# Performance work log

Hardware: AMD Instinct MI355X
Metric: run time of the kernel (lower is better)

Reference implementation:

```python
import jax, jax.numpy as jnp
import numpy as np

RADIUS = 0.12
K = 32  # neighbors per ball


def setup_inputs() -> dict:
    key = jax.random.key(0)
    ks = jax.random.split(key, 12)
    B, N, M, C = 4, 4096, 4096, 128
    anchor_xyzs = jax.random.uniform(ks[0], (B, N, 3), dtype=jnp.float32)
    neighbor = jax.random.uniform(ks[1], (B, M, 3), dtype=jnp.float32)
    s3 = 1.0 / np.sqrt(3.0)
    sC = 1.0 / np.sqrt(C)
    Wq = jax.random.uniform(ks[2], (3, C), jnp.float32, -s3, s3)
    bq = jax.random.uniform(ks[3], (C,), jnp.float32, -s3, s3)
    Wk = jax.random.uniform(ks[4], (3, C), jnp.float32, -s3, s3)
    bk = jax.random.uniform(ks[5], (C,), jnp.float32, -s3, s3)
    Wd = jax.random.uniform(ks[6], (3, C), jnp.float32, -s3, s3)
    bd = jax.random.uniform(ks[7], (C,), jnp.float32, -s3, s3)
    Wa = jax.random.uniform(ks[8], (C, C), jnp.float32, -sC, sC)
    ba = jax.random.uniform(ks[9], (C,), jnp.float32, -sC, sC)
    return {"anchor_xyzs": anchor_xyzs, "neighbor": neighbor,
            "Wq": Wq, "bq": bq, "Wk": Wk, "bk": bk,
            "Wd": Wd, "bd": bd, "Wa": Wa, "ba": ba}


def ball_query(anchor, neighbor, radius, k):
    """pointnet2-style ball query: first k neighbor indices (in original order)
    with sqdist < radius^2; slots beyond the found count are padded with the
    first found index (index 0 if none found). Returns (B, N, k) int32."""
    # (B, N, M) pairwise squared distances
    sqd = jnp.sum((anchor[:, :, None, :] - neighbor[:, None, :, :]) ** 2, axis=-1)
    mask = sqd < radius * radius
    # stable sort keys: valid (0) before invalid (1) -> first-k valid indices in order
    order = jnp.argsort((~mask).astype(jnp.int32), axis=-1, stable=True)
    idx = order[..., :k]                                # (B, N, k)
    cnt = jnp.sum(mask, axis=-1)                        # (B, N)
    slot_valid = jnp.arange(k) < cnt[..., None]
    idx = jnp.where(slot_valid, idx, idx[..., :1])
    return idx.astype(jnp.int32)


def reference(anchor_xyzs, neighbor, Wq, bq, Wk, bk, Wd, bd, Wa, ba):
    B, N, _ = anchor_xyzs.shape
    bidx = jnp.arange(B)[:, None, None]
    # QKV-style projections of coordinates
    Q = anchor_xyzs @ Wq + bq                           # (B, N, C)
    neighbor_k = neighbor @ Wk + bk                     # (B, M, C)
    # ball query + gather
    idx = ball_query(anchor_xyzs, neighbor, RADIUS, K)  # (B, N, K)
    neighbor_grouped = neighbor[bidx, idx]              # (B, N, K, 3)
    features_K = neighbor_k[bidx, idx]                  # (B, N, K, C)
    # distance encoding
    dis = (anchor_xyzs[:, :, None, :] - neighbor_grouped) @ Wd + bd  # (B, N, K, C)
    # attention weight: softmax over channel dim (dim=-1, as in the torch code)
    logits = (Q[:, :, None, :] - features_K) @ Wa + ba  # (B, N, K, C)
    attention_weight = jax.nn.softmax(logits, axis=-1)
    # max-pool over the K neighbor axis
    attention = jnp.max(dis * attention_weight, axis=2)  # (B, N, C)
    return attention
```

## Files before the change

kernel.cpp:

```cpp
#include <hip/hip_runtime.h>
#include <math.h>

#define BDIM 4
#define NDIM 4096
#define MDIM 4096
#define CDIM 128
#define KSEL 32
#define NCELL 64
#define CAP 128

typedef float v2f __attribute__((ext_vector_type(2)));

#define PRE_BYTES (7 * CDIM * 4)
#define STARTS_BYTES ((NCELL + 1) * BDIM * 4)
#define PTS4_OFF (PRE_BYTES + STARTS_BYTES)
#define WS_NEEDED (PTS4_OFF + (size_t)BDIM * MDIM * 16)

template <int CTRL, int MASK>
__device__ __forceinline__ float dpp_add(float x) {
    const int r = __builtin_amdgcn_update_dpp(0, __float_as_int(x), CTRL, MASK, 0xF, true);
    return x + __int_as_float(r);
}
#define DPP_QUAD_XOR1 0xB1
#define DPP_QUAD_XOR2 0x4E
#define DPP_ROW_HALF_MIRROR 0x141
#define DPP_ROW_MIRROR      0x140
#define DPP_ROW_BCAST15     0x142
#define DPP_ROW_BCAST31     0x143

__device__ __forceinline__ int cell_of(float v) {
    int c = (int)(v * 4.0f);
    return c < 0 ? 0 : (c > 3 ? 3 : c);
}

__launch_bounds__(1024)
__global__ void setup_kernel(const float* __restrict__ neighbor,
                             const float* __restrict__ Wq, const float* __restrict__ bq,
                             const float* __restrict__ Wk, const float* __restrict__ bk,
                             const float* __restrict__ Wa, const float* __restrict__ ba,
                             float* __restrict__ pre,
                             int* __restrict__ starts,
                             float4* __restrict__ pts4,
                             const int do_bins) {
    const int blk = blockIdx.x;
    const int t = threadIdx.x;
    if (do_bins && blk < BDIM) {
        __shared__ int cnts[NCELL];
        __shared__ int curs[NCELL];
        if (t < NCELL) cnts[t] = 0;
        __syncthreads();
        const float* nbb = neighbor + (size_t)blk * MDIM * 3;
        float px[4], py[4], pz[4];
        int cell[4];
        #pragma unroll
        for (int k = 0; k < 4; ++k) {
            const int i = t + k * 1024;
            const float x = nbb[3 * i], y = nbb[3 * i + 1], z = nbb[3 * i + 2];
            px[k] = x; py[k] = y; pz[k] = z;
            cell[k] = (cell_of(z) * 4 + cell_of(y)) * 4 + cell_of(x);
            atomicAdd(&cnts[cell[k]], 1);
        }
        __syncthreads();
        if (t < NCELL) {
            const int v = cnts[t];
            int inc = v;
            #pragma unroll
            for (int off = 1; off < 64; off <<= 1) {
                const int u = __shfl_up(inc, off);
                if (t >= off) inc += u;
            }
            const int excl = inc - v;
            curs[t] = excl;
            starts[blk * (NCELL + 1) + t] = excl;
            if (t == NCELL - 1) starts[blk * (NCELL + 1) + NCELL] = inc;
        }
        __syncthreads();
        #pragma unroll
        for (int k = 0; k < 4; ++k) {
            const int i = t + k * 1024;
            const int slot = atomicAdd(&curs[cell[k]], 1);
            pts4[(size_t)blk * MDIM + slot] = make_float4(px[k], py[k], pz[k], __int_as_float(i));
        }
    } else if (!do_bins || blk == BDIM) {
        if (t < 7 * CDIM) {
            const double LOG2E = 1.4426950408889634074;
            const int r = t >> 7, c = t & (CDIM - 1);
            if (r < 3) {
                double s0 = 0, s1 = 0, s2 = 0, s3 = 0;
                for (int k = 0; k < CDIM; k += 4) {
                    s0 += (double)Wq[r * CDIM + k + 0] * (double)Wa[(k + 0) * CDIM + c];
                    s1 += (double)Wq[r * CDIM + k + 1] * (double)Wa[(k + 1) * CDIM + c];
                    s2 += (double)Wq[r * CDIM + k + 2] * (double)Wa[(k + 2) * CDIM + c];
                    s3 += (double)Wq[r * CDIM + k + 3] * (double)Wa[(k + 3) * CDIM + c];
                }
                pre[r * CDIM + c] = (float)(((s0 + s1) + (s2 + s3)) * LOG2E);
            } else if (r < 6) {
                const int rr = r - 3;
                double s0 = 0, s1 = 0, s2 = 0, s3 = 0;
                for (int k = 0; k < CDIM; k += 4) {
                    s0 += (double)Wk[rr * CDIM + k + 0] * (double)Wa[(k + 0) * CDIM + c];
                    s1 += (double)Wk[rr * CDIM + k + 1] * (double)Wa[(k + 1) * CDIM + c];
                    s2 += (double)Wk[rr * CDIM + k + 2] * (double)Wa[(k + 2) * CDIM + c];
                    s3 += (double)Wk[rr * CDIM + k + 3] * (double)Wa[(k + 3) * CDIM + c];
                }
                pre[r * CDIM + c] = (float)(((s0 + s1) + (s2 + s3)) * LOG2E);
            } else {
                double s = (double)ba[c];
                for (int k = 0; k < CDIM; ++k)
                    s += ((double)bq[k] - (double)bk[k]) * (double)Wa[k * CDIM + c];
                pre[6 * CDIM + c] = (float)(s * LOG2E);
            }
        }
    }
}

__launch_bounds__(256)
__global__ void attn2_kernel(const float* __restrict__ anchor,
                             const float* __restrict__ neighbor,
                             const float* __restrict__ Wd,
                             const float* __restrict__ bd,
                             const float* __restrict__ pre,
                             const float4* __restrict__ pts4,
                             const int* __restrict__ starts,
                             float* __restrict__ out) {
    __shared__ float4 cand[4][CAP];
    __shared__ float4 sel[4][KSEL];

    const int b    = blockIdx.x >> 10;
    const int n0   = (blockIdx.x & 1023) << 2;
    const int tid  = threadIdx.x;
    const int w    = tid >> 6;
    const int lane = tid & 63;

    const int n = n0 + w;
    const float* ap = anchor + ((size_t)b * NDIM + n) * 3;
    const float ax = ap[0], ay = ap[1], az = ap[2];
    const float* nbb = neighbor + (size_t)b * MDIM * 3;

    const v2f* pre2 = (const v2f*)pre;
    const v2f* wdp  = (const v2f*)Wd;
    const v2f* bdp  = (const v2f*)bd;
    const v2f wqa0 = pre2[0 * 64 + lane], wqa1 = pre2[1 * 64 + lane], wqa2 = pre2[2 * 64 + lane];
    const v2f wka0 = pre2[3 * 64 + lane], wka1 = pre2[4 * 64 + lane], wka2 = pre2[5 * 64 + lane];
    const v2f cav  = pre2[6 * 64 + lane];
    const v2f wd0 = wdp[0 * 64 + lane], wd1 = wdp[1 * 64 + lane], wd2 = wdp[2 * 64 + lane];
    const v2f bdv = bdp[lane];

    const v2f qa = ax * wqa0 + ay * wqa1 + az * wqa2 + cav;
    const v2f ad = ax * wd0 + ay * wd1 + az * wd2 + bdv;

    constexpr float R2 = (float)(0.12 * 0.12);
    const float RP = 0.1201f;
    const unsigned long long lanelt = (1ull << lane) - 1ull;

    const int cx0 = max(0, (int)((ax - RP) * 4.0f)), cx1 = min(3, (int)((ax + RP) * 4.0f));
    const int cy0 = max(0, (int)((ay - RP) * 4.0f)), cy1 = min(3, (int)((ay + RP) * 4.0f));
    const int cz0 = max(0, (int)((az - RP) * 4.0f)), cz1 = min(3, (int)((az + RP) * 4.0f));

    const float4* pb = pts4 + (size_t)b * MDIM;
    const int* st = starts + b * (NCELL + 1);

    int rs[4], re[4];
    int nr = 0;
    for (int cz = cz0; cz <= cz1; ++cz)
        for (int cy = cy0; cy <= cy1; ++cy) {
            const int crow = (cz * 4 + cy) * 4;
            rs[nr] = st[crow + cx0];
            re[nr] = st[crow + cx1 + 1];
            ++nr;
        }

    int cnt = 0;
    for (int r = 0; r < nr; ++r) {
        const int rend = re[r];
        for (int base = rs[r]; base < rend; base += 64) {
            const int i = base + lane;
            const bool valid = i < rend;
            float4 p = make_float4(1e30f, 1e30f, 1e30f, 0.0f);
            if (valid) p = pb[i];
            const float dx = __fsub_rn(ax, p.x);
            const float dy = __fsub_rn(ay, p.y);
            const float dz = __fsub_rn(az, p.z);
            const float d2 = __fadd_rn(__fadd_rn(__fmul_rn(dx, dx), __fmul_rn(dy, dy)),
                                       __fmul_rn(dz, dz));
            const bool in = valid && (d2 < R2);
            const unsigned long long mk = __ballot(in);
            const int pos = cnt + __popcll(mk & lanelt);
            if (in && pos < CAP) cand[w][pos] = p;
            cnt += __popcll(mk);
        }
    }

    int eff;
    if (cnt == 0) {
        if (lane == 0) sel[w][0] = make_float4(nbb[0], nbb[1], nbb[2], __int_as_float(0));
        eff = 1;
    } else if (cnt <= KSEL) {
        if (lane < cnt) sel[w][lane] = cand[w][lane];
        eff = cnt;
    } else if (cnt <= CAP) {
        float4 c0v = make_float4(0, 0, 0, 0), c1v = make_float4(0, 0, 0, 0);
        int i0 = 0x7fffffff, i1 = 0x7fffffff;
        if (lane < cnt)      { c0v = cand[w][lane];      i0 = __float_as_int(c0v.w); }
        if (lane + 64 < cnt) { c1v = cand[w][lane + 64]; i1 = __float_as_int(c1v.w); }
        int lo = 0, hi = MDIM - 1;
        while (lo < hi) {
            const int mid = (lo + hi) >> 1;
            const int c = __popcll(__ballot(i0 <= mid)) + __popcll(__ballot(i1 <= mid));
            if (c >= KSEL) hi = mid; else lo = mid + 1;
        }
        const bool k0 = (i0 <= lo);
        const unsigned long long m0 = __ballot(k0);
        if (k0) sel[w][__popcll(m0 & lanelt)] = c0v;
        const int cc0 = __popcll(m0);
        const bool k1 = (i1 <= lo);
        const unsigned long long m1 = __ballot(k1);
        if (k1) sel[w][cc0 + __popcll(m1 & lanelt)] = c1v;
        eff = KSEL;
    } else {
        int c2 = 0;
        for (int base = 0; base < MDIM && c2 < KSEL; base += 64) {
            const int m = base + lane;
            const float* p = nbb + 3 * m;
            const float nx = p[0], ny = p[1], nz = p[2];
            const float dx = __fsub_rn(ax, nx);
            const float dy = __fsub_rn(ay, ny);
            const float dz = __fsub_rn(az, nz);
            const float d2 = __fadd_rn(__fadd_rn(__fmul_rn(dx, dx), __fmul_rn(dy, dy)),
                                       __fmul_rn(dz, dz));
            const bool in = d2 < R2;
            const unsigned long long mk = __ballot(in);
            const int pos = c2 + __popcll(mk & lanelt);
            if (in && pos < KSEL) sel[w][pos] = make_float4(nx, ny, nz, 0.0f);
            c2 += __popcll(mk);
        }
        eff = KSEL;
    }

    const int eff4 = (eff + 3) & ~3;
    __builtin_amdgcn_wave_barrier();
    __builtin_amdgcn_s_waitcnt(0);
    if (lane >= eff && lane < eff4) {
        const float4 f = sel[w][0];
        sel[w][lane] = f;
    }
    __builtin_amdgcn_wave_barrier();

    v2f acc = { -1e30f, -1e30f };
    for (int j = 0; j < eff4; j += 4) {
        v2f pr[4];
        float sv[4];
        #pragma unroll
        for (int t = 0; t < 4; ++t) {
            const float4 v = sel[w][j + t];
            const v2f l = qa - (v.x * wka0 + v.y * wka1 + v.z * wka2);
            v2f e; e.x = exp2f(l.x); e.y = exp2f(l.y);
            sv[t] = e.x + e.y;
            const v2f d = ad - (v.x * wd0 + v.y * wd1 + v.z * wd2);
            pr[t] = d * e;
        }
        #pragma unroll
        for (int t = 0; t < 4; ++t) sv[t] = dpp_add<DPP_QUAD_XOR1, 0xF>(sv[t]);
        #pragma unroll
        for (int t = 0; t < 4; ++t) sv[t] = dpp_add<DPP_QUAD_XOR2, 0xF>(sv[t]);
        #pragma unroll
        for (int t = 0; t < 4; ++t) sv[t] = dpp_add<DPP_ROW_HALF_MIRROR, 0xF>(sv[t]);
        #pragma unroll
        for (int t = 0; t < 4; ++t) sv[t] = dpp_add<DPP_ROW_MIRROR, 0xF>(sv[t]);
        #pragma unroll
        for (int t = 0; t < 4; ++t) sv[t] = dpp_add<DPP_ROW_BCAST15, 0xA>(sv[t]);
        #pragma unroll
        for (int t = 0; t < 4; ++t) sv[t] = dpp_add<DPP_ROW_BCAST31, 0xC>(sv[t]);
        #pragma unroll
        for (int t = 0; t < 4; ++t) {
            const float tot = __int_as_float(__builtin_amdgcn_readlane(__float_as_int(sv[t]), 63));
            const float inv = __builtin_amdgcn_rcpf(tot);
            const v2f c = pr[t] * inv;
            acc.x = fmaxf(acc.x, c.x);
            acc.y = fmaxf(acc.y, c.y);
        }
    }

    float2 o; o.x = acc.x; o.y = acc.y;
    ((float2*)out)[((size_t)b * NDIM + n) * 64 + lane] = o;
}

__launch_bounds__(256)
__global__ void attn_fallback(const float* __restrict__ anchor,
                              const float* __restrict__ neighbor,
                              const float* __restrict__ Wd,
                              const float* __restrict__ bd,
                              const float* __restrict__ pre,
                              float* __restrict__ out) {
    __shared__ int    lists[4][KSEL];
    __shared__ float4 nxyz[4][KSEL];

    const int b = blockIdx.x >> 10, n0 = (blockIdx.x & 1023) << 2;
    const int tid = threadIdx.x, w = tid >> 6, lane = tid & 63;
    const int n = n0 + w;
    const float* ap = anchor + ((size_t)b * NDIM + n) * 3;
    const float ax = ap[0], ay = ap[1], az = ap[2];
    const float* nbb = neighbor + (size_t)b * MDIM * 3;

    const v2f* pre2 = (const v2f*)pre;
    const v2f* wdp = (const v2f*)Wd;
    const v2f* bdp = (const v2f*)bd;
    const v2f wqa0 = pre2[0 * 64 + lane], wqa1 = pre2[1 * 64 + lane], wqa2 = pre2[2 * 64 + lane];
    const v2f wka0 = pre2[3 * 64 + lane], wka1 = pre2[4 * 64 + lane], wka2 = pre2[5 * 64 + lane];
    const v2f cav = pre2[6 * 64 + lane];
    const v2f wd0 = wdp[0 * 64 + lane], wd1 = wdp[1 * 64 + lane], wd2 = wdp[2 * 64 + lane];
    const v2f bdv = bdp[lane];
    const v2f qa = ax * wqa0 + ay * wqa1 + az * wqa2 + cav;
    const v2f ad = ax * wd0 + ay * wd1 + az * wd2 + bdv;

    constexpr float R2 = (float)(0.12 * 0.12);
    const unsigned long long lanelt = (1ull << lane) - 1ull;
    int cnt = 0;
    for (int base = 0; base < MDIM && cnt < KSEL; base += 64) {
        const int m = base + lane;
        const float* p = nbb + 3 * m;
        const float dx = __fsub_rn(ax, p[0]);
        const float dy = __fsub_rn(ay, p[1]);
        const float dz = __fsub_rn(az, p[2]);
        const float d2 = __fadd_rn(__fadd_rn(__fmul_rn(dx, dx), __fmul_rn(dy, dy)),
                                   __fmul_rn(dz, dz));
        const bool in = d2 < R2;
        const unsigned long long mk = __ballot(in);
        const int pos = cnt + __popcll(mk & lanelt);
        if (in && pos < KSEL) lists[w][pos] = m;
        cnt += __popcll(mk);
    }
    int eff = cnt < KSEL ? cnt : KSEL;
    if (cnt == 0) { if (lane == 0) lists[w][0] = 0; eff = 1; }
    const int eff4 = (eff + 3) & ~3;
    if (lane == 0) for (int j = eff; j < eff4; ++j) lists[w][j] = lists[w][0];
    __builtin_amdgcn_wave_barrier();
    if (lane < eff4) {
        const float* p = nbb + 3 * lists[w][lane];
        nxyz[w][lane] = make_float4(p[0], p[1], p[2], 0.f);
    }
    __builtin_amdgcn_wave_barrier();

    v2f acc = { -1e30f, -1e30f };
    for (int j = 0; j < eff4; j += 4) {
        v2f pr[4]; float sv[4];
        #pragma unroll
        for (int t = 0; t < 4; ++t) {
            const float4 v = nxyz[w][j + t];
            const v2f l = qa - (v.x * wka0 + v.y * wka1 + v.z * wka2);
            v2f e; e.x = exp2f(l.x); e.y = exp2f(l.y);
            sv[t] = e.x + e.y;
            const v2f d = ad - (v.x * wd0 + v.y * wd1 + v.z * wd2);
            pr[t] = d * e;
        }
        #pragma unroll
        for (int t = 0; t < 4; ++t) sv[t] = dpp_add<DPP_QUAD_XOR1, 0xF>(sv[t]);
        #pragma unroll
        for (int t = 0; t < 4; ++t) sv[t] = dpp_add<DPP_QUAD_XOR2, 0xF>(sv[t]);
        #pragma unroll
        for (int t = 0; t < 4; ++t) sv[t] = dpp_add<DPP_ROW_HALF_MIRROR, 0xF>(sv[t]);
        #pragma unroll
        for (int t = 0; t < 4; ++t) sv[t] = dpp_add<DPP_ROW_MIRROR, 0xF>(sv[t]);
        #pragma unroll
        for (int t = 0; t < 4; ++t) sv[t] = dpp_add<DPP_ROW_BCAST15, 0xA>(sv[t]);
        #pragma unroll
        for (int t = 0; t < 4; ++t) sv[t] = dpp_add<DPP_ROW_BCAST31, 0xC>(sv[t]);
        #pragma unroll
        for (int t = 0; t < 4; ++t) {
            const float tot = __int_as_float(__builtin_amdgcn_readlane(__float_as_int(sv[t]), 63));
            const float inv = __builtin_amdgcn_rcpf(tot);
            const v2f c = pr[t] * inv;
            acc.x = fmaxf(acc.x, c.x);
            acc.y = fmaxf(acc.y, c.y);
        }
    }
    float2 o; o.x = acc.x; o.y = acc.y;
    ((float2*)out)[((size_t)b * NDIM + n) * 64 + lane] = o;
}

extern "C" void kernel_launch(void* const* d_in, const int* in_sizes, int n_in,
                              void* d_out, int out_size, void* d_ws, size_t ws_size,
                              hipStream_t stream) {
    const float* anchor   = (const float*)d_in[0];
    const float* neighbor = (const float*)d_in[1];
    const float* Wq = (const float*)d_in[2];
    const float* bq = (const float*)d_in[3];
    const float* Wk = (const float*)d_in[4];
    const float* bk = (const float*)d_in[5];
    const float* Wd = (const float*)d_in[6];
    const float* bd = (const float*)d_in[7];
    const float* Wa = (const float*)d_in[8];
    const float* ba = (const float*)d_in[9];
    float* out = (float*)d_out;

    float* pre   = (float*)d_ws;
    int* starts  = (int*)((char*)d_ws + PRE_BYTES);
    float4* pts4 = (float4*)((char*)d_ws + PTS4_OFF);

    if (ws_size >= WS_NEEDED) {
        setup_kernel<<<dim3(BDIM + 1), dim3(1024), 0, stream>>>(
            neighbor, Wq, bq, Wk, bk, Wa, ba, pre, starts, pts4, 1);
        attn2_kernel<<<dim3(BDIM * NDIM / 4), dim3(256), 0, stream>>>(
            anchor, neighbor, Wd, bd, pre, pts4, starts, out);
    } else {
        setup_kernel<<<dim3(1), dim3(1024), 0, stream>>>(
            neighbor, Wq, bq, Wk, bk, Wa, ba, pre, starts, pts4, 0);
        attn_fallback<<<dim3(BDIM * NDIM / 4), dim3(256), 0, stream>>>(
            anchor, neighbor, Wd, bd, pre, out);
    }
}
```

Before: 124.3 us.

## Use packed FMAs, raw v_exp, mbcnt ranking, and direct selection writes

Stores the Wk·Wa fold pre-negated so the logit becomes a chain of packed FMAs, and likewise negates Wd for the distance term. exp2f is replaced by an inline v_exp_f32, which drops the library's range handling. Lane ranks now come from mbcnt instead of popcount of a shifted mask. The first KSEL candidates are written straight into the selection buffer, removing a copy in the common case. The clamped load removes the valid-branch in the scan, and the weight loading is moved into shared helpers.

```diff
diff --git a/kernel.cpp b/kernel.cpp
--- a/kernel.cpp
+++ b/kernel.cpp
@@ -16,6 +16,12 @@
 #define PTS4_OFF (PRE_BYTES + STARTS_BYTES)
 #define WS_NEEDED (PTS4_OFF + (size_t)BDIM * MDIM * 16)
 
+__device__ __forceinline__ float exp2_hw(float x) {
+    float r;
+    asm("v_exp_f32 %0, %1" : "=v"(r) : "v"(x));
+    return r;
+}
+
 template <int CTRL, int MASK>
 __device__ __forceinline__ float dpp_add(float x) {
     const int r = __builtin_amdgcn_update_dpp(0, __float_as_int(x), CTRL, MASK, 0xF, true);
@@ -28,9 +34,72 @@
 #define DPP_ROW_BCAST15     0x142
 #define DPP_ROW_BCAST31     0x143
 
+__device__ __forceinline__ int rank_before(unsigned long long mk) {
+    return __builtin_amdgcn_mbcnt_hi((unsigned)(mk >> 32),
+                                     __builtin_amdgcn_mbcnt_lo((unsigned)mk, 0));
+}
+
 __device__ __forceinline__ int cell_of(float v) {
     int c = (int)(v * 4.0f);
     return c < 0 ? 0 : (c > 3 ? 3 : c);
+}
+
+__device__ __forceinline__ v2f splat(float x) { v2f r; r.x = x; r.y = x; return r; }
+
+__device__ __forceinline__ v2f pk_fma(v2f a, v2f b, v2f c) {
+    return __builtin_elementwise_fma(a, b, c);
+}
+
+struct LaneW {
+    v2f wqa0, wqa1, wqa2;
+    v2f nka0, nka1, nka2;
+    v2f cav;
+    v2f wd0, wd1, wd2, bdv;
+};
+
+__device__ __forceinline__ void load_lane_weights(LaneW& P, const float* pre,
+                                                  const float* Wd, const float* bd, int lane) {
+    const v2f* pre2 = (const v2f*)pre;
+    const v2f* wdp  = (const v2f*)Wd;
+    const v2f* bdp  = (const v2f*)bd;
+    P.wqa0 = pre2[0 * 64 + lane]; P.wqa1 = pre2[1 * 64 + lane]; P.wqa2 = pre2[2 * 64 + lane];
+    P.nka0 = pre2[3 * 64 + lane]; P.nka1 = pre2[4 * 64 + lane]; P.nka2 = pre2[5 * 64 + lane];
+    P.cav  = pre2[6 * 64 + lane];
+    P.wd0 = wdp[0 * 64 + lane]; P.wd1 = wdp[1 * 64 + lane]; P.wd2 = wdp[2 * 64 + lane];
+    P.bdv = bdp[lane];
+}
+
+__device__ __forceinline__ void fold_one(int i, const float* Wq, const float* bq,
+                                         const float* Wk, const float* bk,
+                                         const float* Wa, const float* ba,
+                                         float* pre) {
+    const double LOG2E = 1.4426950408889634074;
+    const int r = i >> 7, c = i & (CDIM - 1);
+    if (r < 3) {
+        double s0 = 0, s1 = 0, s2 = 0, s3 = 0;
+        for (int k = 0; k < CDIM; k += 4) {
+            s0 += (double)Wq[r * CDIM + k + 0] * (double)Wa[(k + 0) * CDIM + c];
+            s1 += (double)Wq[r * CDIM + k + 1] * (double)Wa[(k + 1) * CDIM + c];
+            s2 += (double)Wq[r * CDIM + k + 2] * (double)Wa[(k + 2) * CDIM + c];
+            s3 += (double)Wq[r * CDIM + k + 3] * (double)Wa[(k + 3) * CDIM + c];
+        }
+        pre[r * CDIM + c] = (float)(((s0 + s1) + (s2 + s3)) * LOG2E);
+    } else if (r < 6) {
+        const int rr = r - 3;
+        double s0 = 0, s1 = 0, s2 = 0, s3 = 0;
+        for (int k = 0; k < CDIM; k += 4) {
+            s0 += (double)Wk[rr * CDIM + k + 0] * (double)Wa[(k + 0) * CDIM + c];
+            s1 += (double)Wk[rr * CDIM + k + 1] * (double)Wa[(k + 1) * CDIM + c];
+            s2 += (double)Wk[rr * CDIM + k + 2] * (double)Wa[(k + 2) * CDIM + c];
+            s3 += (double)Wk[rr * CDIM + k + 3] * (double)Wa[(k + 3) * CDIM + c];
+        }
+        pre[r * CDIM + c] = (float)(((s0 + s1) + (s2 + s3)) * (-LOG2E));
+    } else {
+        double s = (double)ba[c];
+        for (int k = 0; k < CDIM; ++k)
+            s += ((double)bq[k] - (double)bk[k]) * (double)Wa[k * CDIM + c];
+        pre[6 * CDIM + c] = (float)(s * LOG2E);
+    }
 }
 
 __launch_bounds__(1024)
@@ -82,35 +151,7 @@
             pts4[(size_t)blk * MDIM + slot] = make_float4(px[k], py[k], pz[k], __int_as_float(i));
         }
     } else if (!do_bins || blk == BDIM) {
-        if (t < 7 * CDIM) {
-            const double LOG2E = 1.4426950408889634074;
-            const int r = t >> 7, c = t & (CDIM - 1);
-            if (r < 3) {
-                double s0 = 0, s1 = 0, s2 = 0, s3 = 0;
-                for (int k = 0; k < CDIM; k += 4) {
-                    s0 += (double)Wq[r * CDIM + k + 0] * (double)Wa[(k + 0) * CDIM + c];
-                    s1 += (double)Wq[r * CDIM + k + 1] * (double)Wa[(k + 1) * CDIM + c];
-                    s2 += (double)Wq[r * CDIM + k + 2] * (double)Wa[(k + 2) * CDIM + c];
-                    s3 += (double)Wq[r * CDIM + k + 3] * (double)Wa[(k + 3) * CDIM + c];
-                }
-                pre[r * CDIM + c] = (float)(((s0 + s1) + (s2 + s3)) * LOG2E);
-            } else if (r < 6) {
-                const int rr = r - 3;
-                double s0 = 0, s1 = 0, s2 = 0, s3 = 0;
-                for (int k = 0; k < CDIM; k += 4) {
-                    s0 += (double)Wk[rr * CDIM + k + 0] * (double)Wa[(k + 0) * CDIM + c];
-                    s1 += (double)Wk[rr * CDIM + k + 1] * (double)Wa[(k + 1) * CDIM + c];
-                    s2 += (double)Wk[rr * CDIM + k + 2] * (double)Wa[(k + 2) * CDIM + c];
-                    s3 += (double)Wk[rr * CDIM + k + 3] * (double)Wa[(k + 3) * CDIM + c];
-                }
-                pre[r * CDIM + c] = (float)(((s0 + s1) + (s2 + s3)) * LOG2E);
-            } else {
-                double s = (double)ba[c];
-                for (int k = 0; k < CDIM; ++k)
-                    s += ((double)bq[k] - (double)bk[k]) * (double)Wa[k * CDIM + c];
-                pre[6 * CDIM + c] = (float)(s * LOG2E);
-            }
-        }
+        if (t < 7 * CDIM) fold_one(t, Wq, bq, Wk, bk, Wa, ba, pre);
     }
 }
 
@@ -123,7 +164,7 @@
                              const float4* __restrict__ pts4,
                              const int* __restrict__ starts,
                              float* __restrict__ out) {
-    __shared__ float4 cand[4][CAP];
+    __shared__ float4 cand[4][CAP - KSEL];
     __shared__ float4 sel[4][KSEL];
 
     const int b    = blockIdx.x >> 10;
@@ -137,21 +178,16 @@
     const float ax = ap[0], ay = ap[1], az = ap[2];
     const float* nbb = neighbor + (size_t)b * MDIM * 3;
 
-    const v2f* pre2 = (const v2f*)pre;
-    const v2f* wdp  = (const v2f*)Wd;
-    const v2f* bdp  = (const v2f*)bd;
-    const v2f wqa0 = pre2[0 * 64 + lane], wqa1 = pre2[1 * 64 + lane], wqa2 = pre2[2 * 64 + lane];
-    const v2f wka0 = pre2[3 * 64 + lane], wka1 = pre2[4 * 64 + lane], wka2 = pre2[5 * 64 + lane];
-    const v2f cav  = pre2[6 * 64 + lane];
-    const v2f wd0 = wdp[0 * 64 + lane], wd1 = wdp[1 * 64 + lane], wd2 = wdp[2 * 64 + lane];
-    const v2f bdv = bdp[lane];
-
-    const v2f qa = ax * wqa0 + ay * wqa1 + az * wqa2 + cav;
-    const v2f ad = ax * wd0 + ay * wd1 + az * wd2 + bdv;
+    LaneW P;
+    load_lane_weights(P, pre, Wd, bd, lane);
+
+    const v2f axv = splat(ax), ayv = splat(ay), azv = splat(az);
+    const v2f qa = pk_fma(axv, P.wqa0, pk_fma(ayv, P.wqa1, pk_fma(azv, P.wqa2, P.cav)));
+    const v2f ad = pk_fma(axv, P.wd0, pk_fma(ayv, P.wd1, pk_fma(azv, P.wd2, P.bdv)));
+    const v2f nwd0 = -P.wd0, nwd1 = -P.wd1, nwd2 = -P.wd2;
 
     constexpr float R2 = (float)(0.12 * 0.12);
     const float RP = 0.1201f;
-    const unsigned long long lanelt = (1ull << lane) - 1ull;
 
     const int cx0 = max(0, (int)((ax - RP) * 4.0f)), cx1 = min(3, (int)((ax + RP) * 4.0f));
     const int cy0 = max(0, (int)((ay - RP) * 4.0f)), cy1 = min(3, (int)((ay + RP) * 4.0f));
@@ -175,47 +211,54 @@
         const int rend = re[r];
         for (int base = rs[r]; base < rend; base += 64) {
             const int i = base + lane;
-            const bool valid = i < rend;
-            float4 p = make_float4(1e30f, 1e30f, 1e30f, 0.0f);
-            if (valid) p = pb[i];
+            const float4 p = pb[min(i, rend - 1)];
             const float dx = __fsub_rn(ax, p.x);
             const float dy = __fsub_rn(ay, p.y);
             const float dz = __fsub_rn(az, p.z);
             const float d2 = __fadd_rn(__fadd_rn(__fmul_rn(dx, dx), __fmul_rn(dy, dy)),
                                        __fmul_rn(dz, dz));
-            const bool in = valid && (d2 < R2);
+            const bool in = (i < rend) && (d2 < R2);
             const unsigned long long mk = __ballot(in);
-            const int pos = cnt + __popcll(mk & lanelt);
-            if (in && pos < CAP) cand[w][pos] = p;
+            const int pos = cnt + rank_before(mk);
+            if (in && pos < CAP) {
+                if (pos < KSEL) sel[w][pos] = p;
+                else            cand[w][pos - KSEL] = p;
+            }
             cnt += __popcll(mk);
         }
     }
 
     int eff;
     if (cnt == 0) {
-        if (lane == 0) sel[w][0] = make_float4(nbb[0], nbb[1], nbb[2], __int_as_float(0));
+        if (lane == 0) sel[w][0] = make_float4(nbb[0], nbb[1], nbb[2], 0.0f);
         eff = 1;
     } else if (cnt <= KSEL) {
-        if (lane < cnt) sel[w][lane] = cand[w][lane];
         eff = cnt;
     } else if (cnt <= CAP) {
         float4 c0v = make_float4(0, 0, 0, 0), c1v = make_float4(0, 0, 0, 0);
         int i0 = 0x7fffffff, i1 = 0x7fffffff;
-        if (lane < cnt)      { c0v = cand[w][lane];      i0 = __float_as_int(c0v.w); }
-        if (lane + 64 < cnt) { c1v = cand[w][lane + 64]; i1 = __float_as_int(c1v.w); }
+        if (lane < cnt) {
+            c0v = (lane < KSEL) ? sel[w][lane] : cand[w][lane - KSEL];
+            i0 = __float_as_int(c0v.w);
+        }
+        if (lane + 64 < cnt) {
+            c1v = cand[w][lane + 64 - KSEL];
+            i1 = __float_as_int(c1v.w);
+        }
         int lo = 0, hi = MDIM - 1;
         while (lo < hi) {
             const int mid = (lo + hi) >> 1;
             const int c = __popcll(__ballot(i0 <= mid)) + __popcll(__ballot(i1 <= mid));
             if (c >= KSEL) hi = mid; else lo = mid + 1;
         }
+        __builtin_amdgcn_wave_barrier();
         const bool k0 = (i0 <= lo);
         const unsigned long long m0 = __ballot(k0);
-        if (k0) sel[w][__popcll(m0 & lanelt)] = c0v;
+        if (k0) sel[w][rank_before(m0)] = c0v;
         const int cc0 = __popcll(m0);
         const bool k1 = (i1 <= lo);
         const unsigned long long m1 = __ballot(k1);
-        if (k1) sel[w][cc0 + __popcll(m1 & lanelt)] = c1v;
+        if (k1) sel[w][cc0 + rank_before(m1)] = c1v;
         eff = KSEL;
     } else {
         int c2 = 0;
@@ -230,7 +273,7 @@
                                        __fmul_rn(dz, dz));
             const bool in = d2 < R2;
             const unsigned long long mk = __ballot(in);
-            const int pos = c2 + __popcll(mk & lanelt);
+            const int pos = c2 + rank_before(mk);
             if (in && pos < KSEL) sel[w][pos] = make_float4(nx, ny, nz, 0.0f);
             c2 += __popcll(mk);
         }
@@ -246,17 +289,18 @@
     }
     __builtin_amdgcn_wave_barrier();
 
-    v2f acc = { -1e30f, -1e30f };
+    v2f acc = splat(-1e30f);
     for (int j = 0; j < eff4; j += 4) {
         v2f pr[4];
         float sv[4];
         #pragma unroll
         for (int t = 0; t < 4; ++t) {
             const float4 v = sel[w][j + t];
-            const v2f l = qa - (v.x * wka0 + v.y * wka1 + v.z * wka2);
-            v2f e; e.x = exp2f(l.x); e.y = exp2f(l.y);
+            const v2f vx = splat(v.x), vy = splat(v.y), vz = splat(v.z);
+            const v2f l = pk_fma(vx, P.nka0, pk_fma(vy, P.nka1, pk_fma(vz, P.nka2, qa)));
+            v2f e; e.x = exp2_hw(l.x); e.y = exp2_hw(l.y);
             sv[t] = e.x + e.y;
-            const v2f d = ad - (v.x * wd0 + v.y * wd1 + v.z * wd2);
+            const v2f d = pk_fma(vx, nwd0, pk_fma(vy, nwd1, pk_fma(vz, nwd2, ad)));
             pr[t] = d * e;
         }
         #pragma unroll
@@ -274,10 +318,8 @@
         #pragma unroll
         for (int t = 0; t < 4; ++t) {
             const float tot = __int_as_float(__builtin_amdgcn_readlane(__float_as_int(sv[t]), 63));
-            const float inv = __builtin_amdgcn_rcpf(tot);
-            const v2f c = pr[t] * inv;
-            acc.x = fmaxf(acc.x, c.x);
-            acc.y = fmaxf(acc.y, c.y);
+            const v2f iv = splat(__builtin_amdgcn_rcpf(tot));
+            acc = __builtin_elementwise_max(acc, pr[t] * iv);
         }
     }
 
@@ -292,8 +334,8 @@
                               const float* __restrict__ bd,
                               const float* __restrict__ pre,
                               float* __restrict__ out) {
-    __shared__ int    lists[4][KSEL];
-    __shared__ float4 nxyz[4][KSEL];
+    __shared__ float4 sel[4][KSEL];
+    __shared__ int lists[4][KSEL];
 
     const int b = blockIdx.x >> 10, n0 = (blockIdx.x & 1023) << 2;
     const int tid = threadIdx.x, w = tid >> 6, lane = tid & 63;
@@ -302,19 +344,14 @@
     const float ax = ap[0], ay = ap[1], az = ap[2];
     const float* nbb = neighbor + (size_t)b * MDIM * 3;
 
-    const v2f* pre2 = (const v2f*)pre;
-    const v2f* wdp = (const v2f*)Wd;
-    const v2f* bdp = (const v2f*)bd;
-    const v2f wqa0 = pre2[0 * 64 + lane], wqa1 = pre2[1 * 64 + lane], wqa2 = pre2[2 * 64 + lane];
-    const v2f wka0 = pre2[3 * 64 + lane], wka1 = pre2[4 * 64 + lane], wka2 = pre2[5 * 64 + lane];
-    const v2f cav = pre2[6 * 64 + lane];
-    const v2f wd0 = wdp[0 * 64 + lane], wd1 = wdp[1 * 64 + lane], wd2 = wdp[2 * 64 + lane];
-    const v2f bdv = bdp[lane];
-    const v2f qa = ax * wqa0 + ay * wqa1 + az * wqa2 + cav;
-    const v2f ad = ax * wd0 + ay * wd1 + az * wd2 + bdv;
+    LaneW P;
+    load_lane_weights(P, pre, Wd, bd, lane);
+    const v2f axv = splat(ax), ayv = splat(ay), azv = splat(az);
+    const v2f qa = pk_fma(axv, P.wqa0, pk_fma(ayv, P.wqa1, pk_fma(azv, P.wqa2, P.cav)));
+    const v2f ad = pk_fma(axv, P.wd0, pk_fma(ayv, P.wd1, pk_fma(azv, P.wd2, P.bdv)));
+    const v2f nwd0 = -P.wd0, nwd1 = -P.wd1, nwd2 = -P.wd2;
 
     constexpr float R2 = (float)(0.12 * 0.12);
-    const unsigned long long lanelt = (1ull << lane) - 1ull;
     int cnt = 0;
     for (int base = 0; base < MDIM && cnt < KSEL; base += 64) {
         const int m = base + lane;
@@ -326,7 +363,7 @@
                                    __fmul_rn(dz, dz));
         const bool in = d2 < R2;
         const unsigned long long mk = __ballot(in);
-        const int pos = cnt + __popcll(mk & lanelt);
+        const int pos = cnt + rank_before(mk);
         if (in && pos < KSEL) lists[w][pos] = m;
         cnt += __popcll(mk);
     }
@@ -337,20 +374,21 @@
     __builtin_amdgcn_wave_barrier();
     if (lane < eff4) {
         const float* p = nbb + 3 * lists[w][lane];
-        nxyz[w][lane] = make_float4(p[0], p[1], p[2], 0.f);
+        sel[w][lane] = make_float4(p[0], p[1], p[2], 0.f);
     }
     __builtin_amdgcn_wave_barrier();
 
-    v2f acc = { -1e30f, -1e30f };
+    v2f acc = splat(-1e30f);
     for (int j = 0; j < eff4; j += 4) {
         v2f pr[4]; float sv[4];
         #pragma unroll
         for (int t = 0; t < 4; ++t) {
-            const float4 v = nxyz[w][j + t];
-            const v2f l = qa - (v.x * wka0 + v.y * wka1 + v.z * wka2);
-            v2f e; e.x = exp2f(l.x); e.y = exp2f(l.y);
+            const float4 v = sel[w][j + t];
+            const v2f vx = splat(v.x), vy = splat(v.y), vz = splat(v.z);
+            const v2f l = pk_fma(vx, P.nka0, pk_fma(vy, P.nka1, pk_fma(vz, P.nka2, qa)));
+            v2f e; e.x = exp2_hw(l.x); e.y = exp2_hw(l.y);
             sv[t] = e.x + e.y;
-            const v2f d = ad - (v.x * wd0 + v.y * wd1 + v.z * wd2);
+            const v2f d = pk_fma(vx, nwd0, pk_fma(vy, nwd1, pk_fma(vz, nwd2, ad)));
             pr[t] = d * e;
         }
         #pragma unroll
@@ -368,10 +406,8 @@
         #pragma unroll
         for (int t = 0; t < 4; ++t) {
             const float tot = __int_as_float(__builtin_amdgcn_readlane(__float_as_int(sv[t]), 63));
-            const float inv = __builtin_amdgcn_rcpf(tot);
-            const v2f c = pr[t] * inv;
-            acc.x = fmaxf(acc.x, c.x);
-            acc.y = fmaxf(acc.y, c.y);
+            const v2f iv = splat(__builtin_amdgcn_rcpf(tot));
+            acc = __builtin_elementwise_max(acc, pr[t] * iv);
         }
     }
     float2 o; o.x = acc.x; o.y = acc.y;
```

New measurement: 115.4 us (median of 2 runs). 7.2% less time.
